# Optimization experiments

Hardware: AMD Instinct MI355X
Metric: run time of the kernel (lower is better)

Reference implementation:

```python
import jax, jax.numpy as jnp
import numpy as np

N_NODES = 50000
N_EDGES = 800000
ND = 64   # node_dim
HD = 128  # hidden_dim
ED = 32   # edge_dim


def setup_inputs() -> dict:
    key = jax.random.key(0)
    ks = jax.random.split(key, 16)
    init = lambda k, shape: (jax.random.normal(k, shape, jnp.float32)
                             / np.float32(np.sqrt(shape[0])))
    h = jax.random.normal(ks[0], (N_NODES, ND), jnp.float32)
    x = jax.random.normal(ks[1], (N_NODES, 3), jnp.float32) * 10.0
    edge_index = jax.random.randint(ks[2], (2, N_EDGES), 0, N_NODES, dtype=jnp.int64)
    # realistic edge distances = actual pairwise distances of sampled edges
    edge_dist = jnp.linalg.norm(x[edge_index[0]] - x[edge_index[1]], axis=-1)
    in_dim = 2 * ND + ED
    return {
        "h": h, "x": x, "edge_index": edge_index, "edge_dist": edge_dist,
        # edge_mlp: Linear(1, ED) -> SiLU -> Linear(ED, ED)
        "We1": init(ks[3], (1, ED)), "be1": jnp.zeros((ED,), jnp.float32),
        "We2": init(ks[4], (ED, ED)), "be2": jnp.zeros((ED,), jnp.float32),
        # node_mlp: Linear(in_dim, HD) -> SiLU -> Linear(HD, ND)
        "Wn1": init(ks[5], (in_dim, HD)), "bn1": jnp.zeros((HD,), jnp.float32),
        "Wn2": init(ks[6], (HD, ND)), "bn2": jnp.zeros((ND,), jnp.float32),
        # coord_mlp: Linear(in_dim, HD) -> SiLU -> Linear(HD, 1, bias=False)
        "Wc1": init(ks[7], (in_dim, HD)), "bc1": jnp.zeros((HD,), jnp.float32),
        "Wc2": init(ks[8], (HD, 1)),
    }


def reference(h, x, edge_index, edge_dist,
              We1, be1, We2, be2,
              Wn1, bn1, Wn2, bn2,
              Wc1, bc1, Wc2):
    n = h.shape[0]
    src, dst = edge_index[0], edge_index[1]
    # edge_mlp on scalar distance -> [E, ED]
    e = jax.nn.silu(edge_dist[:, None] @ We1 + be1) @ We2 + be2
    # gather + concat -> [E, 2*ND + ED]
    m_input = jnp.concatenate([h[src], h[dst], e], axis=-1)
    # node messages [E, ND]
    m = jax.nn.silu(m_input @ Wn1 + bn1) @ Wn2 + bn2
    h_agg = jax.ops.segment_sum(m, dst, num_segments=n)
    # coord update weight [E, 1]
    coord_weight = jax.nn.silu(m_input @ Wc1 + bc1) @ Wc2
    dir_vec = x[src] - x[dst]
    dir_len = jnp.clip(jnp.linalg.norm(dir_vec, axis=-1, keepdims=True), 1e-8)
    coord_update = coord_weight * (dir_vec / dir_len)
    x_agg = jax.ops.segment_sum(coord_update, dst, num_segments=n)
    return h + h_agg, x + x_agg
```

## Files before the change

kernel.cpp:

```cpp
#include <hip/hip_runtime.h>


#define NN 50000
#define NE 800000
#define NDIM 64
#define HDIM 128
#define NTILES (NE / 64)
#define MSTRIDE 168
#define HSTRIDE 136
#define NH (NN * NDIM)
#define NX (NN * 3)

#define WS_WN1P 0
#define WS_WC1P 20480
#define WS_BN1P 40960
#define WS_BC1P 41088
#define WS_HBF_OFF 65536
#define WS_TOTAL_BYTES ((size_t)WS_HBF_OFF * 4 + (size_t)NH * 2)

typedef __bf16 bf16x8 __attribute__((ext_vector_type(8)));
typedef float f32x4 __attribute__((ext_vector_type(4)));
typedef unsigned short ushort8 __attribute__((ext_vector_type(8)));
typedef unsigned short ushort4v __attribute__((ext_vector_type(4)));

__device__ __forceinline__ unsigned short f2bf(float f) {
    union { __bf16 b; unsigned short u; } c;
    c.b = (__bf16)f;
    return c.u;
}
__device__ __forceinline__ float silu(float v) {
    return __fdividef(v, 1.0f + __expf(-v));
}
__device__ __forceinline__ void bar_lds() {
    asm volatile("s_waitcnt lgkmcnt(0)" ::: "memory");
    __builtin_amdgcn_s_barrier();
}
__device__ __forceinline__ bf16x8 ld_frag(const unsigned short* p) {
    union { ushort8 u; bf16x8 v; } c;
    c.u = *(const ushort8*)p;
    return c.v;
}
__device__ __forceinline__ bf16x8 mk_frag(const unsigned short* u) {
    union { ushort8 uu; bf16x8 v; } c;
#pragma unroll
    for (int j = 0; j < 8; ++j) c.uu[j] = u[j];
    return c.v;
}

__global__ __launch_bounds__(256) void prep(
    const float* __restrict__ h, const float* __restrict__ x,
    const float* __restrict__ We2, const float* __restrict__ be2,
    const float* __restrict__ Wn1, const float* __restrict__ bn1,
    const float* __restrict__ Wc1, const float* __restrict__ bc1,
    float* __restrict__ out, float* __restrict__ wsf) {
    const int gtid = blockIdx.x * 256 + threadIdx.x;
    const int G = gridDim.x * 256;

    if (gtid < 41216) {
        if (gtid < 40960) {
            const int path = gtid / 20480;
            const int rem = gtid - path * 20480;
            const int r = rem >> 7, col = rem & 127;
            const float* W = path ? Wc1 : Wn1;
            float* Wp = wsf + (path ? WS_WC1P : WS_WN1P);
            if (r < 128) {
                Wp[r * 128 + col] = W[r * 128 + col];
            } else {
                const int j = r - 128;
                float s = 0.0f;
#pragma unroll
                for (int n = 0; n < 32; ++n)
                    s += We2[j * 32 + n] * W[(128 + n) * 128 + col];
                Wp[r * 128 + col] = s;
            }
        } else {
            const int j = gtid - 40960;
            const int path = j >> 7, col = j & 127;
            const float* W = path ? Wc1 : Wn1;
            const float* bb = path ? bc1 : bn1;
            float s = bb[col];
#pragma unroll
            for (int n = 0; n < 32; ++n)
                s += be2[n] * W[(128 + n) * 128 + col];
            wsf[(path ? WS_BC1P : WS_BN1P) + col] = s;
        }
    }

    unsigned short* hbf = (unsigned short*)(wsf + WS_HBF_OFF);
    const float4* h4 = (const float4*)h;
    float4* out4 = (float4*)out;
    for (int i = gtid; i < NH / 4; i += G) {
        const float4 v = h4[i];
        out4[i] = v;
        ushort4v u = { f2bf(v.x), f2bf(v.y), f2bf(v.z), f2bf(v.w) };
        *(ushort4v*)&hbf[i * 4] = u;
    }
    for (int i = gtid; i < NX; i += G) out[NH + i] = x[i];
}

__global__ __launch_bounds__(256, 2) void egnn_edges(
    const float* __restrict__ x,
    const int* __restrict__ srcg, const int* __restrict__ dstg,
    const float* __restrict__ dist,
    const float* __restrict__ We1, const float* __restrict__ be1,
    const float* __restrict__ Wn2, const float* __restrict__ bn2,
    const float* __restrict__ Wc2,
    const float* __restrict__ wsW,
    float* __restrict__ outh, float* __restrict__ outx) {

    __shared__ __align__(16) unsigned short mlds[64 * MSTRIDE];
    __shared__ __align__(16) unsigned short hl[64 * HSTRIDE];
    __shared__ int src_l[64];
    __shared__ int dst_l[64];
    __shared__ float we1_l[32], be1_l[32];
    __shared__ float part_l[256];

    const int tid  = threadIdx.x;
    const int w    = tid >> 6;
    const int lane = tid & 63;
    const int l15  = lane & 15;
    const int quad = lane >> 4;
    const int c4   = tid & 15, sub = tid >> 4;

    const unsigned short* hbf = (const unsigned short*)(wsW + WS_HBF_OFF);
    const float* Wn1p = wsW + WS_WN1P;
    const float* Wc1p = wsW + WS_WC1P;
    const float* bn1p = wsW + WS_BN1P;
    const float* bc1p = wsW + WS_BC1P;

    if (tid < 32) { we1_l[tid] = We1[tid]; be1_l[tid] = be1[tid]; }

    bf16x8 wn1f[5][2], wc1f[5][2];
#pragma unroll
    for (int kc = 0; kc < 5; ++kc) {
#pragma unroll
        for (int nt = 0; nt < 2; ++nt) {
            unsigned short un[8], uc[8];
            const int n = w * 32 + nt * 16 + l15;
#pragma unroll
            for (int j = 0; j < 8; ++j) {
                const int k = kc * 32 + quad * 8 + j;
                un[j] = f2bf(Wn1p[k * HDIM + n]);
                uc[j] = f2bf(Wc1p[k * HDIM + n]);
            }
            wn1f[kc][nt] = mk_frag(un);
            wc1f[kc][nt] = mk_frag(uc);
        }
    }
    bf16x8 wn2f[4];
#pragma unroll
    for (int kc = 0; kc < 4; ++kc) {
        unsigned short u[8];
        const int n = w * 16 + l15;
#pragma unroll
        for (int j = 0; j < 8; ++j) {
            const int k = kc * 32 + quad * 8 + j;
            const int D = (k & ~31) + ((k & 1) << 4) + ((k & 31) >> 1);
            u[j] = f2bf(Wn2[D * NDIM + n]);
        }
        wn2f[kc] = mk_frag(u);
    }
    const float biasN0 = bn1p[w * 32 + l15];
    const float biasN1 = bn1p[w * 32 + 16 + l15];
    const float biasC0 = bc1p[w * 32 + l15];
    const float biasC1 = bc1p[w * 32 + 16 + l15];
    const float bias2v = bn2[w * 16 + l15];
    const float wcA = Wc2[w * 32 + l15];
    const float wcB = Wc2[w * 32 + 16 + l15];

    int psn[4], pdn[4];
    float pdist;
    int psl = 0, pdl = 0;
    ushort4v pus[4], pud[4];
    {
        const int e0 = blockIdx.x * 64;
#pragma unroll
        for (int it = 0; it < 4; ++it) {
            psn[it] = srcg[e0 + sub + it * 16];
            pdn[it] = dstg[e0 + sub + it * 16];
        }
        pdist = dist[e0 + (tid >> 2)];
        if (tid < 64) { psl = srcg[e0 + tid]; pdl = dstg[e0 + tid]; }
#pragma unroll
        for (int it = 0; it < 4; ++it) {
            pus[it] = *(const ushort4v*)(hbf + (size_t)psn[it] * NDIM + c4 * 4);
            pud[it] = *(const ushort4v*)(hbf + (size_t)pdn[it] * NDIM + c4 * 4);
        }
    }

    for (int tile = blockIdx.x; tile < NTILES; tile += gridDim.x) {
        bar_lds();

        float xs0 = 0, xs1 = 0, xs2 = 0, xd0 = 0, xd1 = 0, xd2 = 0;
        if (tid < 64) {
            src_l[tid] = psl; dst_l[tid] = pdl;
            xs0 = x[psl * 3 + 0]; xs1 = x[psl * 3 + 1]; xs2 = x[psl * 3 + 2];
            xd0 = x[pdl * 3 + 0]; xd1 = x[pdl * 3 + 1]; xd2 = x[pdl * 3 + 2];
        }
#pragma unroll
        for (int it = 0; it < 4; ++it) {
            const int el = sub + it * 16;
            *(ushort4v*)&mlds[el * MSTRIDE + c4 * 4] = pus[it];
            *(ushort4v*)&mlds[el * MSTRIDE + 64 + c4 * 4] = pud[it];
        }
        {
            const int el = tid >> 2, j0 = (tid & 3) * 8;
            ushort8 u;
#pragma unroll
            for (int j = 0; j < 8; ++j)
                u[j] = f2bf(silu(pdist * we1_l[j0 + j] + be1_l[j0 + j]));
            *(ushort8*)&mlds[el * MSTRIDE + 128 + j0] = u;
        }
        bar_lds();

        {
            const int tn = tile + (int)gridDim.x;
            const int eb = (tn < NTILES ? tn : tile) * 64;
#pragma unroll
            for (int it = 0; it < 4; ++it) {
                psn[it] = srcg[eb + sub + it * 16];
                pdn[it] = dstg[eb + sub + it * 16];
            }
            pdist = dist[eb + (tid >> 2)];
            if (tid < 64) { psl = srcg[eb + tid]; pdl = dstg[eb + tid]; }
        }

        f32x4 accN[4][2], accC[4][2];
#pragma unroll
        for (int mt = 0; mt < 4; ++mt) {
            accN[mt][0] = (f32x4){biasN0, biasN0, biasN0, biasN0};
            accN[mt][1] = (f32x4){biasN1, biasN1, biasN1, biasN1};
            accC[mt][0] = (f32x4){biasC0, biasC0, biasC0, biasC0};
            accC[mt][1] = (f32x4){biasC1, biasC1, biasC1, biasC1};
        }
#pragma unroll
        for (int kc = 0; kc < 5; ++kc) {
            bf16x8 af[4];
#pragma unroll
            for (int mt = 0; mt < 4; ++mt)
                af[mt] = ld_frag(&mlds[(mt * 16 + l15) * MSTRIDE + kc * 32 + quad * 8]);
#pragma unroll
            for (int mt = 0; mt < 4; ++mt) {
#pragma unroll
                for (int nt = 0; nt < 2; ++nt) {
                    accN[mt][nt] = __builtin_amdgcn_mfma_f32_16x16x32_bf16(
                        af[mt], wn1f[kc][nt], accN[mt][nt], 0, 0, 0);
                    accC[mt][nt] = __builtin_amdgcn_mfma_f32_16x16x32_bf16(
                        af[mt], wc1f[kc][nt], accC[mt][nt], 0, 0, 0);
                }
            }
        }

#pragma unroll
        for (int it = 0; it < 4; ++it) {
            pus[it] = *(const ushort4v*)(hbf + (size_t)psn[it] * NDIM + c4 * 4);
            pud[it] = *(const ushort4v*)(hbf + (size_t)pdn[it] * NDIM + c4 * 4);
        }

        {
            unsigned int* hlu = (unsigned int*)hl;
#pragma unroll
            for (int mt = 0; mt < 4; ++mt)
#pragma unroll
                for (int r = 0; r < 4; ++r) {
                    const unsigned int u0 = f2bf(silu(accN[mt][0][r]));
                    const unsigned int u1 = f2bf(silu(accN[mt][1][r]));
                    hlu[(mt * 16 + quad * 4 + r) * (HSTRIDE / 2) + w * 16 + l15] =
                        (u1 << 16) | u0;
                }
        }

        {
            float p[16];
#pragma unroll
            for (int mt = 0; mt < 4; ++mt)
#pragma unroll
                for (int r = 0; r < 4; ++r)
                    p[mt * 4 + r] = silu(accC[mt][0][r]) * wcA + silu(accC[mt][1][r]) * wcB;

            float q8[8];
#pragma unroll
            for (int i = 0; i < 8; ++i) {
                const float send = (l15 & 8) ? p[i] : p[i + 8];
                const float recv = __shfl_xor(send, 8, 64);
                q8[i] = ((l15 & 8) ? p[i + 8] : p[i]) + recv;
            }
            float q4[4];
#pragma unroll
            for (int i = 0; i < 4; ++i) {
                const float send = (l15 & 4) ? q8[i] : q8[i + 4];
                const float recv = __shfl_xor(send, 4, 64);
                q4[i] = ((l15 & 4) ? q8[i + 4] : q8[i]) + recv;
            }
            float q2[2];
#pragma unroll
            for (int i = 0; i < 2; ++i) {
                const float send = (l15 & 2) ? q4[i] : q4[i + 2];
                const float recv = __shfl_xor(send, 2, 64);
                q2[i] = ((l15 & 2) ? q4[i + 2] : q4[i]) + recv;
            }
            {
                const float send = (l15 & 1) ? q2[0] : q2[1];
                const float recv = __shfl_xor(send, 1, 64);
                const float tot = ((l15 & 1) ? q2[1] : q2[0]) + recv;
                const int edge = (l15 >> 2) * 16 + quad * 4 + (l15 & 3);
                part_l[w * 64 + edge] = tot;
            }
        }
        bar_lds();

        {
            f32x4 acc2[4];
#pragma unroll
            for (int mt = 0; mt < 4; ++mt) acc2[mt] = (f32x4){bias2v, bias2v, bias2v, bias2v};
#pragma unroll
            for (int kc = 0; kc < 4; ++kc) {
#pragma unroll
                for (int mt = 0; mt < 4; ++mt) {
                    bf16x8 a2 = ld_frag(&hl[(mt * 16 + l15) * HSTRIDE + kc * 32 + quad * 8]);
                    acc2[mt] = __builtin_amdgcn_mfma_f32_16x16x32_bf16(a2, wn2f[kc], acc2[mt], 0, 0, 0);
                }
            }
#pragma unroll
            for (int mt = 0; mt < 4; ++mt) {
#pragma unroll
                for (int r = 0; r < 4; ++r) {
                    const int el = mt * 16 + quad * 4 + r;
                    atomicAdd(outh + (size_t)dst_l[el] * NDIM + w * 16 + l15, acc2[mt][r]);
                }
            }
        }

        if (tid < 64) {
            const float cw = part_l[tid] + part_l[64 + tid] + part_l[128 + tid] + part_l[192 + tid];
            const float dx = xs0 - xd0;
            const float dy = xs1 - xd1;
            const float dz = xs2 - xd2;
            float len = sqrtf(dx * dx + dy * dy + dz * dz);
            len = fmaxf(len, 1e-8f);
            const float f = cw / len;
            const int dn = dst_l[tid];
            atomicAdd(outx + (size_t)dn * 3 + 0, f * dx);
            atomicAdd(outx + (size_t)dn * 3 + 1, f * dy);
            atomicAdd(outx + (size_t)dn * 3 + 2, f * dz);
        }
    }
}

extern "C" void kernel_launch(void* const* d_in, const int* in_sizes, int n_in,
                              void* d_out, int out_size, void* d_ws, size_t ws_size,
                              hipStream_t stream) {
    const float* h    = (const float*)d_in[0];
    const float* x    = (const float*)d_in[1];
    const int*   ei   = (const int*)d_in[2];
    const float* dist = (const float*)d_in[3];
    const float* We1  = (const float*)d_in[4];
    const float* be1  = (const float*)d_in[5];
    const float* We2  = (const float*)d_in[6];
    const float* be2  = (const float*)d_in[7];
    const float* Wn1  = (const float*)d_in[8];
    const float* bn1  = (const float*)d_in[9];
    const float* Wn2  = (const float*)d_in[10];
    const float* bn2  = (const float*)d_in[11];
    const float* Wc1  = (const float*)d_in[12];
    const float* bc1  = (const float*)d_in[13];
    const float* Wc2  = (const float*)d_in[14];

    float* out = (float*)d_out;
    float* ws  = (float*)d_ws;

    prep<<<2048, 256, 0, stream>>>(h, x, We2, be2, Wn1, bn1, Wc1, bc1, out, ws);
    egnn_edges<<<1024, 256, 0, stream>>>(x, ei, ei + NE, dist,
                                         We1, be1, Wn2, bn2, Wc2, ws,
                                         out, out + NH);
}
```

Measured before the change: 416.5 us.

## Double edge tile to 128 edges and split node/coord GEMMs into phases

Raises the per-block edge tile from 64 to 128, so each block does twice the MFMA work for each set of weight fragments held in registers and for each barrier. The node and coord first-layer GEMMs now run as separate passes over LDS to limit live accumulator registers. The cross-iteration prefetch of gathered h rows into registers is removed; rows are now loaded at the start of each tile, which exposes gather latency. LDS usage roughly doubles, so occupancy at two blocks per CU may suffer.

```diff
diff --git a/kernel.cpp b/kernel.cpp
--- a/kernel.cpp
+++ b/kernel.cpp
@@ -5,7 +5,8 @@
 #define NE 800000
 #define NDIM 64
 #define HDIM 128
-#define NTILES (NE / 64)
+#define TEDGE 128
+#define NTILES (NE / TEDGE)
 #define MSTRIDE 168
 #define HSTRIDE 136
 #define NH (NN * NDIM)
@@ -16,7 +17,6 @@
 #define WS_BN1P 40960
 #define WS_BC1P 41088
 #define WS_HBF_OFF 65536
-#define WS_TOTAL_BYTES ((size_t)WS_HBF_OFF * 4 + (size_t)NH * 2)
 
 typedef __bf16 bf16x8 __attribute__((ext_vector_type(8)));
 typedef float f32x4 __attribute__((ext_vector_type(4)));
@@ -45,6 +45,33 @@
 #pragma unroll
     for (int j = 0; j < 8; ++j) c.uu[j] = u[j];
     return c.v;
+}
+
+__device__ __forceinline__ float butterfly16(const float* p, int l15) {
+    float q8[8];
+#pragma unroll
+    for (int i = 0; i < 8; ++i) {
+        const float send = (l15 & 8) ? p[i] : p[i + 8];
+        const float recv = __shfl_xor(send, 8, 64);
+        q8[i] = ((l15 & 8) ? p[i + 8] : p[i]) + recv;
+    }
+    float q4[4];
+#pragma unroll
+    for (int i = 0; i < 4; ++i) {
+        const float send = (l15 & 4) ? q8[i] : q8[i + 4];
+        const float recv = __shfl_xor(send, 4, 64);
+        q4[i] = ((l15 & 4) ? q8[i + 4] : q8[i]) + recv;
+    }
+    float q2[2];
+#pragma unroll
+    for (int i = 0; i < 2; ++i) {
+        const float send = (l15 & 2) ? q4[i] : q4[i + 2];
+        const float recv = __shfl_xor(send, 2, 64);
+        q2[i] = ((l15 & 2) ? q4[i + 2] : q4[i]) + recv;
+    }
+    const float send = (l15 & 1) ? q2[0] : q2[1];
+    const float recv = __shfl_xor(send, 1, 64);
+    return ((l15 & 1) ? q2[1] : q2[0]) + recv;
 }
 
 __global__ __launch_bounds__(256) void prep(
@@ -108,19 +135,19 @@
     const float* __restrict__ wsW,
     float* __restrict__ outh, float* __restrict__ outx) {
 
-    __shared__ __align__(16) unsigned short mlds[64 * MSTRIDE];
-    __shared__ __align__(16) unsigned short hl[64 * HSTRIDE];
-    __shared__ int src_l[64];
-    __shared__ int dst_l[64];
+    __shared__ __align__(16) unsigned short mlds[TEDGE * MSTRIDE];
+    __shared__ __align__(16) unsigned short hl[TEDGE * HSTRIDE];
+    __shared__ int src_l[TEDGE];
+    __shared__ int dst_l[TEDGE];
     __shared__ float we1_l[32], be1_l[32];
-    __shared__ float part_l[256];
+    __shared__ float part_l[4 * TEDGE];
 
     const int tid  = threadIdx.x;
     const int w    = tid >> 6;
     const int lane = tid & 63;
     const int l15  = lane & 15;
     const int quad = lane >> 4;
-    const int c4   = tid & 15, sub = tid >> 4;
+    const int c4   = tid & 15, sub16 = tid >> 4;
 
     const unsigned short* hbf = (const unsigned short*)(wsW + WS_HBF_OFF);
     const float* Wn1p = wsW + WS_WN1P;
@@ -168,99 +195,88 @@
     const float wcA = Wc2[w * 32 + l15];
     const float wcB = Wc2[w * 32 + 16 + l15];
 
-    int psn[4], pdn[4];
+    int psn[8], pdn[8];
     float pdist;
     int psl = 0, pdl = 0;
-    ushort4v pus[4], pud[4];
     {
-        const int e0 = blockIdx.x * 64;
-#pragma unroll
-        for (int it = 0; it < 4; ++it) {
-            psn[it] = srcg[e0 + sub + it * 16];
-            pdn[it] = dstg[e0 + sub + it * 16];
-        }
-        pdist = dist[e0 + (tid >> 2)];
-        if (tid < 64) { psl = srcg[e0 + tid]; pdl = dstg[e0 + tid]; }
-#pragma unroll
-        for (int it = 0; it < 4; ++it) {
-            pus[it] = *(const ushort4v*)(hbf + (size_t)psn[it] * NDIM + c4 * 4);
-            pud[it] = *(const ushort4v*)(hbf + (size_t)pdn[it] * NDIM + c4 * 4);
-        }
+        const int e0 = blockIdx.x * TEDGE;
+#pragma unroll
+        for (int it = 0; it < 8; ++it) {
+            psn[it] = srcg[e0 + sub16 + it * 16];
+            pdn[it] = dstg[e0 + sub16 + it * 16];
+        }
+        pdist = dist[e0 + (tid >> 1)];
+        if (tid < 128) { psl = srcg[e0 + tid]; pdl = dstg[e0 + tid]; }
     }
 
     for (int tile = blockIdx.x; tile < NTILES; tile += gridDim.x) {
         bar_lds();
 
         float xs0 = 0, xs1 = 0, xs2 = 0, xd0 = 0, xd1 = 0, xd2 = 0;
-        if (tid < 64) {
+        if (tid < 128) {
             src_l[tid] = psl; dst_l[tid] = pdl;
             xs0 = x[psl * 3 + 0]; xs1 = x[psl * 3 + 1]; xs2 = x[psl * 3 + 2];
             xd0 = x[pdl * 3 + 0]; xd1 = x[pdl * 3 + 1]; xd2 = x[pdl * 3 + 2];
         }
-#pragma unroll
-        for (int it = 0; it < 4; ++it) {
-            const int el = sub + it * 16;
-            *(ushort4v*)&mlds[el * MSTRIDE + c4 * 4] = pus[it];
-            *(ushort4v*)&mlds[el * MSTRIDE + 64 + c4 * 4] = pud[it];
-        }
-        {
-            const int el = tid >> 2, j0 = (tid & 3) * 8;
-            ushort8 u;
+        {
+            ushort4v us[8], ud[8];
+#pragma unroll
+            for (int it = 0; it < 8; ++it) {
+                us[it] = *(const ushort4v*)(hbf + (size_t)psn[it] * NDIM + c4 * 4);
+                ud[it] = *(const ushort4v*)(hbf + (size_t)pdn[it] * NDIM + c4 * 4);
+            }
+#pragma unroll
+            for (int it = 0; it < 8; ++it) {
+                const int el = sub16 + it * 16;
+                *(ushort4v*)&mlds[el * MSTRIDE + c4 * 4] = us[it];
+                *(ushort4v*)&mlds[el * MSTRIDE + 64 + c4 * 4] = ud[it];
+            }
+        }
+        {
+            const int el = tid >> 1, j0 = (tid & 1) * 16;
+            ushort8 ua, ub;
 #pragma unroll
             for (int j = 0; j < 8; ++j)
-                u[j] = f2bf(silu(pdist * we1_l[j0 + j] + be1_l[j0 + j]));
-            *(ushort8*)&mlds[el * MSTRIDE + 128 + j0] = u;
+                ua[j] = f2bf(silu(pdist * we1_l[j0 + j] + be1_l[j0 + j]));
+#pragma unroll
+            for (int j = 0; j < 8; ++j)
+                ub[j] = f2bf(silu(pdist * we1_l[j0 + 8 + j] + be1_l[j0 + 8 + j]));
+            *(ushort8*)&mlds[el * MSTRIDE + 128 + j0] = ua;
+            *(ushort8*)&mlds[el * MSTRIDE + 128 + j0 + 8] = ub;
         }
         bar_lds();
 
         {
             const int tn = tile + (int)gridDim.x;
-            const int eb = (tn < NTILES ? tn : tile) * 64;
-#pragma unroll
-            for (int it = 0; it < 4; ++it) {
-                psn[it] = srcg[eb + sub + it * 16];
-                pdn[it] = dstg[eb + sub + it * 16];
-            }
-            pdist = dist[eb + (tid >> 2)];
-            if (tid < 64) { psl = srcg[eb + tid]; pdl = dstg[eb + tid]; }
-        }
-
-        f32x4 accN[4][2], accC[4][2];
-#pragma unroll
-        for (int mt = 0; mt < 4; ++mt) {
-            accN[mt][0] = (f32x4){biasN0, biasN0, biasN0, biasN0};
-            accN[mt][1] = (f32x4){biasN1, biasN1, biasN1, biasN1};
-            accC[mt][0] = (f32x4){biasC0, biasC0, biasC0, biasC0};
-            accC[mt][1] = (f32x4){biasC1, biasC1, biasC1, biasC1};
-        }
-#pragma unroll
-        for (int kc = 0; kc < 5; ++kc) {
-            bf16x8 af[4];
-#pragma unroll
-            for (int mt = 0; mt < 4; ++mt)
-                af[mt] = ld_frag(&mlds[(mt * 16 + l15) * MSTRIDE + kc * 32 + quad * 8]);
-#pragma unroll
-            for (int mt = 0; mt < 4; ++mt) {
-#pragma unroll
-                for (int nt = 0; nt < 2; ++nt) {
-                    accN[mt][nt] = __builtin_amdgcn_mfma_f32_16x16x32_bf16(
-                        af[mt], wn1f[kc][nt], accN[mt][nt], 0, 0, 0);
-                    accC[mt][nt] = __builtin_amdgcn_mfma_f32_16x16x32_bf16(
-                        af[mt], wc1f[kc][nt], accC[mt][nt], 0, 0, 0);
-                }
-            }
-        }
-
-#pragma unroll
-        for (int it = 0; it < 4; ++it) {
-            pus[it] = *(const ushort4v*)(hbf + (size_t)psn[it] * NDIM + c4 * 4);
-            pud[it] = *(const ushort4v*)(hbf + (size_t)pdn[it] * NDIM + c4 * 4);
-        }
-
-        {
+            const int eb = (tn < NTILES ? tn : tile) * TEDGE;
+#pragma unroll
+            for (int it = 0; it < 8; ++it) {
+                psn[it] = srcg[eb + sub16 + it * 16];
+                pdn[it] = dstg[eb + sub16 + it * 16];
+            }
+            pdist = dist[eb + (tid >> 1)];
+            if (tid < 128) { psl = srcg[eb + tid]; pdl = dstg[eb + tid]; }
+        }
+
+        {
+            f32x4 accN[8][2];
+#pragma unroll
+            for (int mt = 0; mt < 8; ++mt) {
+                accN[mt][0] = (f32x4){biasN0, biasN0, biasN0, biasN0};
+                accN[mt][1] = (f32x4){biasN1, biasN1, biasN1, biasN1};
+            }
+#pragma unroll
+            for (int kc = 0; kc < 5; ++kc) {
+#pragma unroll
+                for (int mt = 0; mt < 8; ++mt) {
+                    bf16x8 af = ld_frag(&mlds[(mt * 16 + l15) * MSTRIDE + kc * 32 + quad * 8]);
+                    accN[mt][0] = __builtin_amdgcn_mfma_f32_16x16x32_bf16(af, wn1f[kc][0], accN[mt][0], 0, 0, 0);
+                    accN[mt][1] = __builtin_amdgcn_mfma_f32_16x16x32_bf16(af, wn1f[kc][1], accN[mt][1], 0, 0, 0);
+                }
+            }
             unsigned int* hlu = (unsigned int*)hl;
 #pragma unroll
-            for (int mt = 0; mt < 4; ++mt)
+            for (int mt = 0; mt < 8; ++mt)
 #pragma unroll
                 for (int r = 0; r < 4; ++r) {
                     const unsigned int u0 = f2bf(silu(accN[mt][0][r]));
@@ -271,58 +287,51 @@
         }
 
         {
-            float p[16];
+            f32x4 accC[8][2];
+#pragma unroll
+            for (int mt = 0; mt < 8; ++mt) {
+                accC[mt][0] = (f32x4){biasC0, biasC0, biasC0, biasC0};
+                accC[mt][1] = (f32x4){biasC1, biasC1, biasC1, biasC1};
+            }
+#pragma unroll
+            for (int kc = 0; kc < 5; ++kc) {
+#pragma unroll
+                for (int mt = 0; mt < 8; ++mt) {
+                    bf16x8 af = ld_frag(&mlds[(mt * 16 + l15) * MSTRIDE + kc * 32 + quad * 8]);
+                    accC[mt][0] = __builtin_amdgcn_mfma_f32_16x16x32_bf16(af, wc1f[kc][0], accC[mt][0], 0, 0, 0);
+                    accC[mt][1] = __builtin_amdgcn_mfma_f32_16x16x32_bf16(af, wc1f[kc][1], accC[mt][1], 0, 0, 0);
+                }
+            }
+            float pA[16], pB[16];
 #pragma unroll
             for (int mt = 0; mt < 4; ++mt)
 #pragma unroll
-                for (int r = 0; r < 4; ++r)
-                    p[mt * 4 + r] = silu(accC[mt][0][r]) * wcA + silu(accC[mt][1][r]) * wcB;
-
-            float q8[8];
-#pragma unroll
-            for (int i = 0; i < 8; ++i) {
-                const float send = (l15 & 8) ? p[i] : p[i + 8];
-                const float recv = __shfl_xor(send, 8, 64);
-                q8[i] = ((l15 & 8) ? p[i + 8] : p[i]) + recv;
-            }
-            float q4[4];
-#pragma unroll
-            for (int i = 0; i < 4; ++i) {
-                const float send = (l15 & 4) ? q8[i] : q8[i + 4];
-                const float recv = __shfl_xor(send, 4, 64);
-                q4[i] = ((l15 & 4) ? q8[i + 4] : q8[i]) + recv;
-            }
-            float q2[2];
-#pragma unroll
-            for (int i = 0; i < 2; ++i) {
-                const float send = (l15 & 2) ? q4[i] : q4[i + 2];
-                const float recv = __shfl_xor(send, 2, 64);
-                q2[i] = ((l15 & 2) ? q4[i + 2] : q4[i]) + recv;
-            }
-            {
-                const float send = (l15 & 1) ? q2[0] : q2[1];
-                const float recv = __shfl_xor(send, 1, 64);
-                const float tot = ((l15 & 1) ? q2[1] : q2[0]) + recv;
-                const int edge = (l15 >> 2) * 16 + quad * 4 + (l15 & 3);
-                part_l[w * 64 + edge] = tot;
-            }
+                for (int r = 0; r < 4; ++r) {
+                    pA[mt * 4 + r] = silu(accC[mt][0][r]) * wcA + silu(accC[mt][1][r]) * wcB;
+                    pB[mt * 4 + r] = silu(accC[mt + 4][0][r]) * wcA + silu(accC[mt + 4][1][r]) * wcB;
+                }
+            const float totA = butterfly16(pA, l15);
+            const float totB = butterfly16(pB, l15);
+            const int edge = (l15 >> 2) * 16 + quad * 4 + (l15 & 3);
+            part_l[w * 128 + edge] = totA;
+            part_l[w * 128 + 64 + edge] = totB;
         }
         bar_lds();
 
         {
-            f32x4 acc2[4];
-#pragma unroll
-            for (int mt = 0; mt < 4; ++mt) acc2[mt] = (f32x4){bias2v, bias2v, bias2v, bias2v};
+            f32x4 acc2[8];
+#pragma unroll
+            for (int mt = 0; mt < 8; ++mt) acc2[mt] = (f32x4){bias2v, bias2v, bias2v, bias2v};
 #pragma unroll
             for (int kc = 0; kc < 4; ++kc) {
 #pragma unroll
-                for (int mt = 0; mt < 4; ++mt) {
+                for (int mt = 0; mt < 8; ++mt) {
                     bf16x8 a2 = ld_frag(&hl[(mt * 16 + l15) * HSTRIDE + kc * 32 + quad * 8]);
                     acc2[mt] = __builtin_amdgcn_mfma_f32_16x16x32_bf16(a2, wn2f[kc], acc2[mt], 0, 0, 0);
                 }
             }
 #pragma unroll
-            for (int mt = 0; mt < 4; ++mt) {
+            for (int mt = 0; mt < 8; ++mt) {
 #pragma unroll
                 for (int r = 0; r < 4; ++r) {
                     const int el = mt * 16 + quad * 4 + r;
@@ -331,8 +340,8 @@
             }
         }
 
-        if (tid < 64) {
-            const float cw = part_l[tid] + part_l[64 + tid] + part_l[128 + tid] + part_l[192 + tid];
+        if (tid < 128) {
+            const float cw = part_l[tid] + part_l[128 + tid] + part_l[256 + tid] + part_l[384 + tid];
             const float dx = xs0 - xd0;
             const float dy = xs1 - xd1;
             const float dz = xs2 - xd2;
```

New measurement: 470.9 us. 1.13x slower.

## Fuse prep kernel into edge kernel, gather fp32 h directly, init output via atomics

Applied to the files above, without the earlier changes.

Removes the separate prep kernel. Each block now folds We2/be2 into its Wn1/Wc1 fragments and biases itself, and the residual h and x are added into a memset-zeroed output with atomicAdd instead of being copied. Node features are gathered as fp32 straight from h and converted to bf16 per tile, which drops the bf16 staging copy and the register prefetch of the next tile's rows. The trade-off is twice the gather bytes, gather latency that is no longer hidden behind the MFMA work, redundant weight-fold arithmetic in every block, and many extra atomics for the residual.

```diff
diff --git a/kernel.cpp b/kernel.cpp
--- a/kernel.cpp
+++ b/kernel.cpp
@@ -10,13 +10,7 @@
 #define HSTRIDE 136
 #define NH (NN * NDIM)
 #define NX (NN * 3)
-
-#define WS_WN1P 0
-#define WS_WC1P 20480
-#define WS_BN1P 40960
-#define WS_BC1P 41088
-#define WS_HBF_OFF 65536
-#define WS_TOTAL_BYTES ((size_t)WS_HBF_OFF * 4 + (size_t)NH * 2)
+#define GRID 1024
 
 typedef __bf16 bf16x8 __attribute__((ext_vector_type(8)));
 typedef float f32x4 __attribute__((ext_vector_type(4)));
@@ -47,66 +41,17 @@
     return c.v;
 }
 
-__global__ __launch_bounds__(256) void prep(
+__global__ __launch_bounds__(256, 2) void egnn_all(
     const float* __restrict__ h, const float* __restrict__ x,
-    const float* __restrict__ We2, const float* __restrict__ be2,
-    const float* __restrict__ Wn1, const float* __restrict__ bn1,
-    const float* __restrict__ Wc1, const float* __restrict__ bc1,
-    float* __restrict__ out, float* __restrict__ wsf) {
-    const int gtid = blockIdx.x * 256 + threadIdx.x;
-    const int G = gridDim.x * 256;
-
-    if (gtid < 41216) {
-        if (gtid < 40960) {
-            const int path = gtid / 20480;
-            const int rem = gtid - path * 20480;
-            const int r = rem >> 7, col = rem & 127;
-            const float* W = path ? Wc1 : Wn1;
-            float* Wp = wsf + (path ? WS_WC1P : WS_WN1P);
-            if (r < 128) {
-                Wp[r * 128 + col] = W[r * 128 + col];
-            } else {
-                const int j = r - 128;
-                float s = 0.0f;
-#pragma unroll
-                for (int n = 0; n < 32; ++n)
-                    s += We2[j * 32 + n] * W[(128 + n) * 128 + col];
-                Wp[r * 128 + col] = s;
-            }
-        } else {
-            const int j = gtid - 40960;
-            const int path = j >> 7, col = j & 127;
-            const float* W = path ? Wc1 : Wn1;
-            const float* bb = path ? bc1 : bn1;
-            float s = bb[col];
-#pragma unroll
-            for (int n = 0; n < 32; ++n)
-                s += be2[n] * W[(128 + n) * 128 + col];
-            wsf[(path ? WS_BC1P : WS_BN1P) + col] = s;
-        }
-    }
-
-    unsigned short* hbf = (unsigned short*)(wsf + WS_HBF_OFF);
-    const float4* h4 = (const float4*)h;
-    float4* out4 = (float4*)out;
-    for (int i = gtid; i < NH / 4; i += G) {
-        const float4 v = h4[i];
-        out4[i] = v;
-        ushort4v u = { f2bf(v.x), f2bf(v.y), f2bf(v.z), f2bf(v.w) };
-        *(ushort4v*)&hbf[i * 4] = u;
-    }
-    for (int i = gtid; i < NX; i += G) out[NH + i] = x[i];
-}
-
-__global__ __launch_bounds__(256, 2) void egnn_edges(
-    const float* __restrict__ x,
     const int* __restrict__ srcg, const int* __restrict__ dstg,
     const float* __restrict__ dist,
     const float* __restrict__ We1, const float* __restrict__ be1,
+    const float* __restrict__ We2, const float* __restrict__ be2,
+    const float* __restrict__ Wn1, const float* __restrict__ bn1,
     const float* __restrict__ Wn2, const float* __restrict__ bn2,
+    const float* __restrict__ Wc1, const float* __restrict__ bc1,
     const float* __restrict__ Wc2,
-    const float* __restrict__ wsW,
-    float* __restrict__ outh, float* __restrict__ outx) {
+    float* __restrict__ out) {
 
     __shared__ __align__(16) unsigned short mlds[64 * MSTRIDE];
     __shared__ __align__(16) unsigned short hl[64 * HSTRIDE];
@@ -122,13 +67,26 @@
     const int quad = lane >> 4;
     const int c4   = tid & 15, sub = tid >> 4;
 
-    const unsigned short* hbf = (const unsigned short*)(wsW + WS_HBF_OFF);
-    const float* Wn1p = wsW + WS_WN1P;
-    const float* Wc1p = wsW + WS_WC1P;
-    const float* bn1p = wsW + WS_BN1P;
-    const float* bc1p = wsW + WS_BC1P;
+    float* outh = out;
+    float* outx = out + NH;
 
     if (tid < 32) { we1_l[tid] = We1[tid]; be1_l[tid] = be1[tid]; }
+
+    {
+        const int gtid = blockIdx.x * 256 + tid;
+        const int G = GRID * 256;
+        const float4* h4 = (const float4*)h;
+#pragma unroll 1
+        for (int i = gtid; i < NH / 4; i += G) {
+            const float4 v = h4[i];
+            atomicAdd(outh + i * 4 + 0, v.x);
+            atomicAdd(outh + i * 4 + 1, v.y);
+            atomicAdd(outh + i * 4 + 2, v.z);
+            atomicAdd(outh + i * 4 + 3, v.w);
+        }
+#pragma unroll 1
+        for (int i = gtid; i < NX; i += G) atomicAdd(outx + i, x[i]);
+    }
 
     bf16x8 wn1f[5][2], wc1f[5][2];
 #pragma unroll
@@ -140,8 +98,21 @@
 #pragma unroll
             for (int j = 0; j < 8; ++j) {
                 const int k = kc * 32 + quad * 8 + j;
-                un[j] = f2bf(Wn1p[k * HDIM + n]);
-                uc[j] = f2bf(Wc1p[k * HDIM + n]);
+                float vn, vc;
+                if (k < 128) {
+                    vn = Wn1[k * HDIM + n];
+                    vc = Wc1[k * HDIM + n];
+                } else {
+                    const int m = k - 128;
+                    vn = 0.0f; vc = 0.0f;
+#pragma unroll
+                    for (int jj = 0; jj < 32; ++jj) {
+                        const float w2 = We2[m * 32 + jj];
+                        vn += w2 * Wn1[(128 + jj) * HDIM + n];
+                        vc += w2 * Wc1[(128 + jj) * HDIM + n];
+                    }
+                }
+                un[j] = f2bf(vn); uc[j] = f2bf(vc);
             }
             wn1f[kc][nt] = mk_frag(un);
             wc1f[kc][nt] = mk_frag(uc);
@@ -160,10 +131,20 @@
         }
         wn2f[kc] = mk_frag(u);
     }
-    const float biasN0 = bn1p[w * 32 + l15];
-    const float biasN1 = bn1p[w * 32 + 16 + l15];
-    const float biasC0 = bc1p[w * 32 + l15];
-    const float biasC1 = bc1p[w * 32 + 16 + l15];
+    float biasN0, biasN1, biasC0, biasC1;
+    {
+        const int n0 = w * 32 + l15, n1 = n0 + 16;
+        float a0 = bn1[n0], a1 = bn1[n1], b0 = bc1[n0], b1 = bc1[n1];
+#pragma unroll
+        for (int m = 0; m < 32; ++m) {
+            const float bm = be2[m];
+            a0 += bm * Wn1[(128 + m) * HDIM + n0];
+            a1 += bm * Wn1[(128 + m) * HDIM + n1];
+            b0 += bm * Wc1[(128 + m) * HDIM + n0];
+            b1 += bm * Wc1[(128 + m) * HDIM + n1];
+        }
+        biasN0 = a0; biasN1 = a1; biasC0 = b0; biasC1 = b1;
+    }
     const float bias2v = bn2[w * 16 + l15];
     const float wcA = Wc2[w * 32 + l15];
     const float wcB = Wc2[w * 32 + 16 + l15];
@@ -171,7 +152,6 @@
     int psn[4], pdn[4];
     float pdist;
     int psl = 0, pdl = 0;
-    ushort4v pus[4], pud[4];
     {
         const int e0 = blockIdx.x * 64;
 #pragma unroll
@@ -181,11 +161,6 @@
         }
         pdist = dist[e0 + (tid >> 2)];
         if (tid < 64) { psl = srcg[e0 + tid]; pdl = dstg[e0 + tid]; }
-#pragma unroll
-        for (int it = 0; it < 4; ++it) {
-            pus[it] = *(const ushort4v*)(hbf + (size_t)psn[it] * NDIM + c4 * 4);
-            pud[it] = *(const ushort4v*)(hbf + (size_t)pdn[it] * NDIM + c4 * 4);
-        }
     }
 
     for (int tile = blockIdx.x; tile < NTILES; tile += gridDim.x) {
@@ -200,8 +175,12 @@
 #pragma unroll
         for (int it = 0; it < 4; ++it) {
             const int el = sub + it * 16;
-            *(ushort4v*)&mlds[el * MSTRIDE + c4 * 4] = pus[it];
-            *(ushort4v*)&mlds[el * MSTRIDE + 64 + c4 * 4] = pud[it];
+            const float4 hs = *(const float4*)(h + (size_t)psn[it] * NDIM + c4 * 4);
+            const float4 hd = *(const float4*)(h + (size_t)pdn[it] * NDIM + c4 * 4);
+            ushort4v us = { f2bf(hs.x), f2bf(hs.y), f2bf(hs.z), f2bf(hs.w) };
+            ushort4v ud = { f2bf(hd.x), f2bf(hd.y), f2bf(hd.z), f2bf(hd.w) };
+            *(ushort4v*)&mlds[el * MSTRIDE + c4 * 4] = us;
+            *(ushort4v*)&mlds[el * MSTRIDE + 64 + c4 * 4] = ud;
         }
         {
             const int el = tid >> 2, j0 = (tid & 3) * 8;
@@ -249,12 +228,6 @@
                         af[mt], wc1f[kc][nt], accC[mt][nt], 0, 0, 0);
                 }
             }
-        }
-
-#pragma unroll
-        for (int it = 0; it < 4; ++it) {
-            pus[it] = *(const ushort4v*)(hbf + (size_t)psn[it] * NDIM + c4 * 4);
-            pud[it] = *(const ushort4v*)(hbf + (size_t)pdn[it] * NDIM + c4 * 4);
         }
 
         {
@@ -366,11 +339,10 @@
     const float* bc1  = (const float*)d_in[13];
     const float* Wc2  = (const float*)d_in[14];
 
-    float* out = (float*)d_out;
-    float* ws  = (float*)d_ws;
-
-    prep<<<2048, 256, 0, stream>>>(h, x, We2, be2, Wn1, bn1, Wc1, bc1, out, ws);
-    egnn_edges<<<1024, 256, 0, stream>>>(x, ei, ei + NE, dist,
-                                         We1, be1, Wn2, bn2, Wc2, ws,
-                                         out, out + NH);
-}
+    hipMemsetAsync(d_out, 0, (size_t)(NH + NX) * 4, stream);
+    egnn_all<<<GRID, 256, 0, stream>>>(h, x, ei, ei + NE, dist,
+                                       We1, be1, We2, be2,
+                                       Wn1, bn1, Wn2, bn2,
+                                       Wc1, bc1, Wc2,
+                                       (float*)d_out);
+}
```

Result: slower. 928.6 us (+122.9%).
